# Kernel tuning notes

Hardware: AMD Instinct MI355X
Metric: run time of the kernel (lower is better)

The kernel has to match this reference:

```python
import jax, jax.numpy as jnp
import numpy as np

N_NODES = 100000
N_EDGES = 1600000
F_IN = 64
HID = 64
N_ACT = 8


def gcn_conv(x, edge_index, W, b):
    # PyG GCNConv: h = x @ W; add self-loops; norm = deg^{-1/2}[src]*deg^{-1/2}[dst];
    # out[dst] += norm * h[src]; out += b
    n = x.shape[0]
    h = x @ W  # [N, out]
    row = jnp.concatenate([edge_index[0], jnp.arange(n)])  # src (+ self loops)
    col = jnp.concatenate([edge_index[1], jnp.arange(n)])  # dst (+ self loops)
    deg = jax.ops.segment_sum(jnp.ones_like(col, dtype=h.dtype), col, num_segments=n)
    dinv = jnp.where(deg > 0, jax.lax.rsqrt(deg), 0.0)
    norm = dinv[row] * dinv[col]  # [E+N]
    msg = h[row] * norm[:, None]  # gather + scale
    out = jax.ops.segment_sum(msg, col, num_segments=n)  # scatter-add
    return out + b


def setup_inputs() -> dict:
    key = jax.random.key(0)
    ks = jax.random.split(key, 8)
    x = jax.random.normal(ks[0], (N_NODES, F_IN), dtype=jnp.float32)
    edge_index = jax.random.randint(ks[1], (2, N_EDGES), 0, N_NODES, dtype=jnp.int64)
    def glorot(k, fan_in, fan_out):
        s = jnp.sqrt(6.0 / (fan_in + fan_out))
        return jax.random.uniform(k, (fan_in, fan_out), jnp.float32, -s, s)
    W1 = glorot(ks[2], F_IN, HID)
    b1 = jnp.zeros((HID,), jnp.float32)
    W2 = glorot(ks[3], HID, HID)
    b2 = jnp.zeros((HID,), jnp.float32)
    Wfc = glorot(ks[4], HID, N_ACT)
    bfc = jnp.zeros((N_ACT,), jnp.float32)
    return {"x": x, "edge_index": edge_index, "W1": W1, "b1": b1,
            "W2": W2, "b2": b2, "Wfc": Wfc, "bfc": bfc}


def reference(x, edge_index, W1, b1, W2, b2, Wfc, bfc):
    h = jax.nn.relu(gcn_conv(x, edge_index, W1, b1))
    h = jax.nn.relu(gcn_conv(h, edge_index, W2, b2))
    return h @ Wfc + bfc  # Q-values per node: [N, num_actions]
```

## Files before the change

### kernel.cpp

```cpp
#include <hip/hip_runtime.h>
#include <hip/hip_fp16.h>


#define F 64
#define NACT 8
#define BSH 9
#define BNODES 512
#define CAP 10240
#define EPB 2048
#define HS 67

__global__ __launch_bounds__(256) void k_init(const unsigned int* __restrict__ w,
    int* flag, int* cursor, int E) {
  if (threadIdx.x == 0) *flag = 1;
  cursor[threadIdx.x] = 0;
  __syncthreads();
  int bad = 0;
  for (int i = threadIdx.x; i < 8192; i += 256) {
    if (i < E && w[2 * i + 1] != 0u) bad = 1;
  }
  if (bad) atomicAnd(flag, 0);
}

__device__ __forceinline__ int edge_row(const unsigned int* w, int flag, int e, int E) {
  return flag ? (int)w[2 * e] : (int)w[e];
}
__device__ __forceinline__ int edge_col(const unsigned int* w, int flag, int e, int E) {
  return flag ? (int)w[2 * E + 2 * e] : (int)w[E + e];
}

__global__ __launch_bounds__(256) void k_scatterE(const unsigned int* __restrict__ w,
    const int* __restrict__ flag, int* __restrict__ cursor, unsigned int* __restrict__ slab, int E) {
  __shared__ int hist[256];
  __shared__ int base[256];
  const int tid = threadIdx.x;
  const int fl = *flag;
  hist[tid] = 0;
  __syncthreads();
  int pk[8], bb[8], lr[8];
  const int e0 = blockIdx.x * EPB;
#pragma unroll 8
  for (int j = 0; j < 8; ++j) {
    int e = e0 + j * 256 + tid;
    bb[j] = -1;
    if (e < E) {
      int c = edge_col(w, fl, e, E);
      int s = edge_row(w, fl, e, E);
      int b = c >> BSH;
      pk[j] = (unsigned)s | ((unsigned)(c & (BNODES - 1)) << 17);
      bb[j] = b;
      lr[j] = atomicAdd(&hist[b], 1);
    }
  }
  __syncthreads();
  int h = hist[tid];
  if (h > 0) base[tid] = atomicAdd(&cursor[tid], h);
  __syncthreads();
#pragma unroll 8
  for (int j = 0; j < 8; ++j) {
    if (bb[j] >= 0) {
      slab[(size_t)bb[j] * CAP + base[bb[j]] + lr[j]] = (unsigned)pk[j];
    }
  }
}

__global__ __launch_bounds__(64) void k_slabscan(const int* __restrict__ cursor,
    int* __restrict__ bucketBase, int* __restrict__ csr_off, int NB, int n, int E) {
  int t = threadIdx.x;
  int per = (NB + 63) / 64;
  int base = t * per;
  int local = 0;
  for (int i = 0; i < per; ++i) if (base + i < NB) local += cursor[base + i];
  int inc = local;
  for (int off = 1; off < 64; off <<= 1) {
    int vv = __shfl_up(inc, off);
    if (t >= off) inc += vv;
  }
  int run = inc - local;
  for (int i = 0; i < per; ++i) if (base + i < NB) { bucketBase[base + i] = run; run += cursor[base + i]; }
  if (t == 63) { bucketBase[NB] = inc; csr_off[n] = E; }
}

__global__ __launch_bounds__(256) void k_bucketcsr(const unsigned int* __restrict__ slab,
    const int* __restrict__ bucketBase, int* __restrict__ csr_off, float* __restrict__ dinv,
    int* __restrict__ csr_src, int n) {
  __shared__ int cnt[BNODES];
  __shared__ int off[BNODES];
  __shared__ int sA[256], sB[256];
  const int tid = threadIdx.x;
  const int b = blockIdx.x;
  const int csrbeg = bucketBase[b];
  const int cntb = bucketBase[b + 1] - csrbeg;
  const unsigned int* sl = &slab[(size_t)b * CAP];
  cnt[tid] = 0;
  cnt[tid + 256] = 0;
  __syncthreads();
  for (int i = tid; i < cntb; i += 256) {
    atomicAdd(&cnt[sl[i] >> 17], 1);
  }
  __syncthreads();
  int c0 = cnt[2 * tid], c1 = cnt[2 * tid + 1];
  int p = c0 + c1;
  sA[tid] = p;
  __syncthreads();
  int* srcb = sA;
  int* dstb = sB;
  for (int o = 1; o < 256; o <<= 1) {
    int v = srcb[tid];
    if (tid >= o) v += srcb[tid - o];
    __syncthreads();
    dstb[tid] = v;
    __syncthreads();
    int* t2 = srcb; srcb = dstb; dstb = t2;
  }
  int ex2 = srcb[tid] - p;
  off[2 * tid] = ex2;
  off[2 * tid + 1] = ex2 + c0;
  __syncthreads();
  int v0 = (b << BSH) + 2 * tid;
  if (v0 < n) { csr_off[v0] = csrbeg + off[2 * tid]; dinv[v0] = rsqrtf((float)(c0 + 1)); }
  if (v0 + 1 < n) { csr_off[v0 + 1] = csrbeg + off[2 * tid + 1]; dinv[v0 + 1] = rsqrtf((float)(c1 + 1)); }
  __syncthreads();
  for (int i = tid; i < cntb; i += 256) {
    unsigned int pk = sl[i];
    int dl = pk >> 17;
    int pos = atomicAdd(&off[dl], 1);
    csr_src[csrbeg + pos] = (int)(pk & 0x1FFFFu);
  }
}

__device__ __forceinline__ ushort4 packh4(float a, float b, float c, float d) {
  ushort4 r;
  r.x = __half_as_ushort(__float2half_rn(a));
  r.y = __half_as_ushort(__float2half_rn(b));
  r.z = __half_as_ushort(__float2half_rn(c));
  r.w = __half_as_ushort(__float2half_rn(d));
  return r;
}

__device__ __forceinline__ void accmix(float* a, uint4 g) {
  float one = 1.0f;
  asm volatile(
    "v_fma_mix_f32 %0, %9, %8, %0 op_sel:[0,0,0] op_sel_hi:[1,0,0]\n\t"
    "v_fma_mix_f32 %1, %9, %8, %1 op_sel:[1,0,0] op_sel_hi:[1,0,0]\n\t"
    "v_fma_mix_f32 %2, %10, %8, %2 op_sel:[0,0,0] op_sel_hi:[1,0,0]\n\t"
    "v_fma_mix_f32 %3, %10, %8, %3 op_sel:[1,0,0] op_sel_hi:[1,0,0]\n\t"
    "v_fma_mix_f32 %4, %11, %8, %4 op_sel:[0,0,0] op_sel_hi:[1,0,0]\n\t"
    "v_fma_mix_f32 %5, %11, %8, %5 op_sel:[1,0,0] op_sel_hi:[1,0,0]\n\t"
    "v_fma_mix_f32 %6, %12, %8, %6 op_sel:[0,0,0] op_sel_hi:[1,0,0]\n\t"
    "v_fma_mix_f32 %7, %12, %8, %7 op_sel:[1,0,0] op_sel_hi:[1,0,0]"
    : "+v"(a[0]), "+v"(a[1]), "+v"(a[2]), "+v"(a[3]),
      "+v"(a[4]), "+v"(a[5]), "+v"(a[6]), "+v"(a[7])
    : "v"(one), "v"(g.x), "v"(g.y), "v"(g.z), "v"(g.w));
}

__device__ __forceinline__ void gather8(const uint4* __restrict__ Gv,
    const int* __restrict__ csr_src, int beg, int end, int l, float* a) {
  int j = beg;
  for (; j + 8 <= end; j += 8) {
    uint4 g0 = Gv[(size_t)csr_src[j + 0] * 8 + l];
    uint4 g1 = Gv[(size_t)csr_src[j + 1] * 8 + l];
    uint4 g2 = Gv[(size_t)csr_src[j + 2] * 8 + l];
    uint4 g3 = Gv[(size_t)csr_src[j + 3] * 8 + l];
    uint4 g4 = Gv[(size_t)csr_src[j + 4] * 8 + l];
    uint4 g5 = Gv[(size_t)csr_src[j + 5] * 8 + l];
    uint4 g6 = Gv[(size_t)csr_src[j + 6] * 8 + l];
    uint4 g7 = Gv[(size_t)csr_src[j + 7] * 8 + l];
    accmix(a, g0); accmix(a, g1); accmix(a, g2); accmix(a, g3);
    accmix(a, g4); accmix(a, g5); accmix(a, g6); accmix(a, g7);
  }
  for (; j + 4 <= end; j += 4) {
    uint4 g0 = Gv[(size_t)csr_src[j + 0] * 8 + l];
    uint4 g1 = Gv[(size_t)csr_src[j + 1] * 8 + l];
    uint4 g2 = Gv[(size_t)csr_src[j + 2] * 8 + l];
    uint4 g3 = Gv[(size_t)csr_src[j + 3] * 8 + l];
    accmix(a, g0); accmix(a, g1); accmix(a, g2); accmix(a, g3);
  }
  for (; j < end; ++j) accmix(a, Gv[(size_t)csr_src[j] * 8 + l]);
}

__global__ __launch_bounds__(256) void k_gemm_h(const float* __restrict__ X, const float* __restrict__ W,
    const float* __restrict__ dinv, unsigned short* __restrict__ Gh, int n) {
  __shared__ float xst[F * 68];
  __shared__ float wsh[F * F];
  const int tid = threadIdx.x;
  const int row0 = blockIdx.x * 64;
  for (int i = tid * 4; i < F * F; i += 1024)
    *(float4*)&wsh[i] = *(const float4*)&W[i];
  for (int i = tid * 4; i < 64 * F; i += 1024) {
    int r = i >> 6, k = i & 63;
    float4 v = make_float4(0.f, 0.f, 0.f, 0.f);
    if (row0 + r < n) v = *(const float4*)&X[(size_t)(row0 + r) * F + k];
    xst[(k + 0) * 68 + r] = v.x;
    xst[(k + 1) * 68 + r] = v.y;
    xst[(k + 2) * 68 + r] = v.z;
    xst[(k + 3) * 68 + r] = v.w;
  }
  __syncthreads();
  const int tc = tid & 15;
  const int tr = tid >> 4;
  float a00 = 0.f, a01 = 0.f, a02 = 0.f, a03 = 0.f;
  float a10 = 0.f, a11 = 0.f, a12 = 0.f, a13 = 0.f;
  float a20 = 0.f, a21 = 0.f, a22 = 0.f, a23 = 0.f;
  float a30 = 0.f, a31 = 0.f, a32 = 0.f, a33 = 0.f;
  const float* xp = &xst[tr * 4];
  const float* wp = &wsh[tc * 4];
#pragma unroll 8
  for (int k = 0; k < F; ++k) {
    float4 xv = *(const float4*)&xp[k * 68];
    float4 wv = *(const float4*)&wp[k * F];
    a00 = fmaf(xv.x, wv.x, a00); a01 = fmaf(xv.x, wv.y, a01);
    a02 = fmaf(xv.x, wv.z, a02); a03 = fmaf(xv.x, wv.w, a03);
    a10 = fmaf(xv.y, wv.x, a10); a11 = fmaf(xv.y, wv.y, a11);
    a12 = fmaf(xv.y, wv.z, a12); a13 = fmaf(xv.y, wv.w, a13);
    a20 = fmaf(xv.z, wv.x, a20); a21 = fmaf(xv.z, wv.y, a21);
    a22 = fmaf(xv.z, wv.z, a22); a23 = fmaf(xv.z, wv.w, a23);
    a30 = fmaf(xv.w, wv.x, a30); a31 = fmaf(xv.w, wv.y, a31);
    a32 = fmaf(xv.w, wv.z, a32); a33 = fmaf(xv.w, wv.w, a33);
  }
  const int gc = tc * 4;
  int gr = row0 + tr * 4;
  if (gr + 0 < n) { float d = dinv[gr + 0]; *(ushort4*)&Gh[(size_t)(gr + 0) * F + gc] = packh4(a00 * d, a01 * d, a02 * d, a03 * d); }
  if (gr + 1 < n) { float d = dinv[gr + 1]; *(ushort4*)&Gh[(size_t)(gr + 1) * F + gc] = packh4(a10 * d, a11 * d, a12 * d, a13 * d); }
  if (gr + 2 < n) { float d = dinv[gr + 2]; *(ushort4*)&Gh[(size_t)(gr + 2) * F + gc] = packh4(a20 * d, a21 * d, a22 * d, a23 * d); }
  if (gr + 3 < n) { float d = dinv[gr + 3]; *(ushort4*)&Gh[(size_t)(gr + 3) * F + gc] = packh4(a30 * d, a31 * d, a32 * d, a33 * d); }
}

__global__ __launch_bounds__(512) void k_gather_gemm(const int* __restrict__ csr_off,
    const int* __restrict__ csr_src, const unsigned short* __restrict__ Gh1,
    const float* __restrict__ dinv, const float* __restrict__ bias,
    const float* __restrict__ W2, unsigned short* __restrict__ Gh2, int n) {
  __shared__ float hst[F * HS];
  __shared__ float wsh[F * F];
  const int tid = threadIdx.x;
  const int row0 = blockIdx.x * 64;
  {
    int i = tid * 8;
    *(float4*)&wsh[i] = *(const float4*)&W2[i];
    *(float4*)&wsh[i + 4] = *(const float4*)&W2[i + 4];
  }
  const int ln = tid >> 3;
  const int l = tid & 7;
  const int v = row0 + ln;
  float a[8] = {0.f, 0.f, 0.f, 0.f, 0.f, 0.f, 0.f, 0.f};
  if (v < n) {
    const uint4* Gv = (const uint4*)Gh1;
    accmix(a, Gv[(size_t)v * 8 + l]);
    gather8(Gv, csr_src, csr_off[v], csr_off[v + 1], l, a);
    float d = dinv[v];
#pragma unroll
    for (int jj = 0; jj < 8; ++jj) {
      float h = fmaxf(fmaf(a[jj], d, bias[l * 8 + jj]), 0.f);
      hst[(l * 8 + jj) * HS + ln] = h;
    }
  } else {
#pragma unroll
    for (int jj = 0; jj < 8; ++jj) hst[(l * 8 + jj) * HS + ln] = 0.f;
  }
  __syncthreads();
  const int tc = tid & 15;
  const int tr = tid >> 4;
  const int r0 = 2 * tr;
  float a00 = 0.f, a01 = 0.f, a02 = 0.f, a03 = 0.f;
  float a10 = 0.f, a11 = 0.f, a12 = 0.f, a13 = 0.f;
  const float* wp = &wsh[tc * 4];
#pragma unroll 8
  for (int k = 0; k < F; ++k) {
    float h0 = hst[k * HS + r0];
    float h1 = hst[k * HS + r0 + 1];
    float4 wv = *(const float4*)&wp[k * F];
    a00 = fmaf(h0, wv.x, a00); a01 = fmaf(h0, wv.y, a01);
    a02 = fmaf(h0, wv.z, a02); a03 = fmaf(h0, wv.w, a03);
    a10 = fmaf(h1, wv.x, a10); a11 = fmaf(h1, wv.y, a11);
    a12 = fmaf(h1, wv.z, a12); a13 = fmaf(h1, wv.w, a13);
  }
  const int gc = tc * 4;
  int gr = row0 + r0;
  if (gr < n) { float d = dinv[gr]; *(ushort4*)&Gh2[(size_t)gr * F + gc] = packh4(a00 * d, a01 * d, a02 * d, a03 * d); }
  if (gr + 1 < n) { float d = dinv[gr + 1]; *(ushort4*)&Gh2[(size_t)(gr + 1) * F + gc] = packh4(a10 * d, a11 * d, a12 * d, a13 * d); }
}

__global__ __launch_bounds__(256) void k_gather_fc(const int* __restrict__ csr_off,
    const int* __restrict__ csr_src, const unsigned short* __restrict__ Gh,
    const float* __restrict__ dinv, const float* __restrict__ bias,
    const float* __restrict__ Wfc, const float* __restrict__ bfc,
    float* __restrict__ OUT, int n) {
  __shared__ float wsh[F * 9];
  __shared__ float bs[NACT];
  const int tid = threadIdx.x;
  for (int i = tid; i < F * NACT; i += 256) wsh[(i >> 3) * 9 + (i & 7)] = Wfc[i];
  if (tid < NACT) bs[tid] = bfc[tid];
  __syncthreads();
  int v = blockIdx.x * 32 + (tid >> 3);
  int l = tid & 7;
  if (v >= n) return;
  const uint4* Gv = (const uint4*)Gh;
  float a[8] = {0.f, 0.f, 0.f, 0.f, 0.f, 0.f, 0.f, 0.f};
  accmix(a, Gv[(size_t)v * 8 + l]);
  gather8(Gv, csr_src, csr_off[v], csr_off[v + 1], l, a);
  float d = dinv[v];
  float q[NACT] = {0.f, 0.f, 0.f, 0.f, 0.f, 0.f, 0.f, 0.f};
#pragma unroll
  for (int jj = 0; jj < 8; ++jj) {
    float h = fmaxf(fmaf(a[jj], d, bias[l * 8 + jj]), 0.f);
    const float* wr = &wsh[(l * 8 + jj) * 9];
#pragma unroll
    for (int aa = 0; aa < NACT; ++aa) q[aa] = fmaf(h, wr[aa], q[aa]);
  }
#pragma unroll
  for (int m = 1; m < 8; m <<= 1) {
#pragma unroll
    for (int aa = 0; aa < NACT; ++aa) q[aa] += __shfl_xor(q[aa], m);
  }
  OUT[(size_t)v * NACT + l] = q[l] + bs[l];
}

extern "C" void kernel_launch(void* const* d_in, const int* in_sizes, int n_in,
                              void* d_out, int out_size, void* d_ws, size_t ws_size,
                              hipStream_t stream) {
  const float* x = (const float*)d_in[0];
  const unsigned int* ew = (const unsigned int*)d_in[1];
  const float* W1 = (const float*)d_in[2];
  const float* b1 = (const float*)d_in[3];
  const float* W2 = (const float*)d_in[4];
  const float* b2 = (const float*)d_in[5];
  const float* Wfc = (const float*)d_in[6];
  const float* bfc = (const float*)d_in[7];
  float* out = (float*)d_out;
  const int n = in_sizes[0] / F;
  const int E = in_sizes[1] / 2;
  const int NB = (n + BNODES - 1) >> BSH;

  char* base = (char*)d_ws;
  size_t off = 0;
  auto alloc = [&](size_t bytes) { void* p = base + off; off += (bytes + 255) & ~(size_t)255; return p; };
  int* flag = (int*)alloc(4);
  int* cursor = (int*)alloc(256 * 4);
  int* bucketBase = (int*)alloc((size_t)(NB + 1) * 4);
  int* csr_off = (int*)alloc((size_t)(n + 1) * 4);
  float* dinv = (float*)alloc((size_t)n * 4);
  unsigned int* slab = (unsigned int*)alloc((size_t)NB * CAP * 4);
  int* csr_src = (int*)alloc((size_t)E * 4);
  unsigned short* Gh1 = (unsigned short*)alloc((size_t)n * F * 2);
  unsigned short* Gh2 = (unsigned short*)alloc((size_t)n * F * 2);

  const int gbSc = (E + EPB - 1) / EPB;
  const int gbRow = (n + 63) / 64;
  const int gbGa = (n + 31) / 32;

  hipLaunchKernelGGL(k_init, dim3(1), dim3(256), 0, stream, ew, flag, cursor, E);
  hipLaunchKernelGGL(k_scatterE, dim3(gbSc), dim3(256), 0, stream, ew, flag, cursor, slab, E);
  hipLaunchKernelGGL(k_slabscan, dim3(1), dim3(64), 0, stream, cursor, bucketBase, csr_off, NB, n, E);
  hipLaunchKernelGGL(k_bucketcsr, dim3(NB), dim3(256), 0, stream, slab, bucketBase, csr_off, dinv, csr_src, n);

  hipLaunchKernelGGL(k_gemm_h, dim3(gbRow), dim3(256), 0, stream, x, W1, dinv, Gh1, n);
  hipLaunchKernelGGL(k_gather_gemm, dim3(gbRow), dim3(512), 0, stream, csr_off, csr_src, Gh1, dinv, b1, W2, Gh2, n);
  hipLaunchKernelGGL(k_gather_fc, dim3(gbGa), dim3(256), 0, stream, csr_off, csr_src, Gh2, dinv, b2, Wfc, bfc, out, n);
}
```

Measured before the change: 163.6 us.

## Edge-balanced gather with shared-memory atomics and fold slab scan into bucket CSR

Each gather block now spreads its 64 nodes' incoming edges evenly across its 64 thread groups. It uses a binary search over shared CSR offsets and accumulates partial sums into shared memory with atomics, instead of giving one node to each 8-lane group. This targets load imbalance from varying degrees. The separate single-block scan kernel is removed, and every bucket-CSR block recomputes the prefix over bucket counts itself, saving one launch. The fc gather now uses 512-thread blocks over 64 nodes. The cost is extra shared-memory atomics, extra syncs and fp32 accumulation of the self term via unpacking.

Result: slower. 283.9 us (+73.5%).

```diff
diff --git a/kernel.cpp b/kernel.cpp
--- a/kernel.cpp
+++ b/kernel.cpp
@@ -9,6 +9,7 @@
 #define CAP 10240
 #define EPB 2048
 #define HS 67
+#define ACCS 69
 
 __global__ __launch_bounds__(256) void k_init(const unsigned int* __restrict__ w,
     int* flag, int* cursor, int E) {
@@ -64,44 +65,17 @@
   }
 }
 
-__global__ __launch_bounds__(64) void k_slabscan(const int* __restrict__ cursor,
-    int* __restrict__ bucketBase, int* __restrict__ csr_off, int NB, int n, int E) {
-  int t = threadIdx.x;
-  int per = (NB + 63) / 64;
-  int base = t * per;
-  int local = 0;
-  for (int i = 0; i < per; ++i) if (base + i < NB) local += cursor[base + i];
-  int inc = local;
-  for (int off = 1; off < 64; off <<= 1) {
-    int vv = __shfl_up(inc, off);
-    if (t >= off) inc += vv;
-  }
-  int run = inc - local;
-  for (int i = 0; i < per; ++i) if (base + i < NB) { bucketBase[base + i] = run; run += cursor[base + i]; }
-  if (t == 63) { bucketBase[NB] = inc; csr_off[n] = E; }
-}
-
 __global__ __launch_bounds__(256) void k_bucketcsr(const unsigned int* __restrict__ slab,
-    const int* __restrict__ bucketBase, int* __restrict__ csr_off, float* __restrict__ dinv,
-    int* __restrict__ csr_src, int n) {
+    const int* __restrict__ cursor, int* __restrict__ csr_off, float* __restrict__ dinv,
+    int* __restrict__ csr_src, int n, int NB, int E) {
   __shared__ int cnt[BNODES];
   __shared__ int off[BNODES];
   __shared__ int sA[256], sB[256];
+  __shared__ int sMeta[2];
   const int tid = threadIdx.x;
   const int b = blockIdx.x;
-  const int csrbeg = bucketBase[b];
-  const int cntb = bucketBase[b + 1] - csrbeg;
-  const unsigned int* sl = &slab[(size_t)b * CAP];
-  cnt[tid] = 0;
-  cnt[tid + 256] = 0;
-  __syncthreads();
-  for (int i = tid; i < cntb; i += 256) {
-    atomicAdd(&cnt[sl[i] >> 17], 1);
-  }
-  __syncthreads();
-  int c0 = cnt[2 * tid], c1 = cnt[2 * tid + 1];
-  int p = c0 + c1;
-  sA[tid] = p;
+  int cv = (tid < NB) ? cursor[tid] : 0;
+  sA[tid] = cv;
   __syncthreads();
   int* srcb = sA;
   int* dstb = sB;
@@ -113,6 +87,32 @@
     __syncthreads();
     int* t2 = srcb; srcb = dstb; dstb = t2;
   }
+  if (tid == b) { sMeta[0] = srcb[b] - cv; sMeta[1] = cv; }
+  if (b == 0 && tid == 0) csr_off[n] = E;
+  __syncthreads();
+  const int csrbeg = sMeta[0];
+  const int cntb = sMeta[1];
+  const unsigned int* sl = &slab[(size_t)b * CAP];
+  cnt[tid] = 0;
+  cnt[tid + 256] = 0;
+  __syncthreads();
+  for (int i = tid; i < cntb; i += 256) {
+    atomicAdd(&cnt[sl[i] >> 17], 1);
+  }
+  __syncthreads();
+  int c0 = cnt[2 * tid], c1 = cnt[2 * tid + 1];
+  int p = c0 + c1;
+  sA[tid] = p;
+  __syncthreads();
+  srcb = sA; dstb = sB;
+  for (int o = 1; o < 256; o <<= 1) {
+    int v = srcb[tid];
+    if (tid >= o) v += srcb[tid - o];
+    __syncthreads();
+    dstb[tid] = v;
+    __syncthreads();
+    int* t2 = srcb; srcb = dstb; dstb = t2;
+  }
   int ex2 = srcb[tid] - p;
   off[2 * tid] = ex2;
   off[2 * tid + 1] = ex2 + c0;
@@ -136,6 +136,17 @@
   r.z = __half_as_ushort(__float2half_rn(c));
   r.w = __half_as_ushort(__float2half_rn(d));
   return r;
+}
+
+__device__ __forceinline__ void unpack8(uint4 g, float* f) {
+  union { uint4 u; __half2 h[4]; } u;
+  u.u = g;
+#pragma unroll
+  for (int i = 0; i < 4; ++i) {
+    float2 t = __half22float2(u.h[i]);
+    f[2 * i] = t.x;
+    f[2 * i + 1] = t.y;
+  }
 }
 
 __device__ __forceinline__ void accmix(float* a, uint4 g) {
@@ -154,29 +165,40 @@
     : "v"(one), "v"(g.x), "v"(g.y), "v"(g.z), "v"(g.w));
 }
 
-__device__ __forceinline__ void gather8(const uint4* __restrict__ Gv,
-    const int* __restrict__ csr_src, int beg, int end, int l, float* a) {
-  int j = beg;
-  for (; j + 8 <= end; j += 8) {
-    uint4 g0 = Gv[(size_t)csr_src[j + 0] * 8 + l];
-    uint4 g1 = Gv[(size_t)csr_src[j + 1] * 8 + l];
-    uint4 g2 = Gv[(size_t)csr_src[j + 2] * 8 + l];
-    uint4 g3 = Gv[(size_t)csr_src[j + 3] * 8 + l];
-    uint4 g4 = Gv[(size_t)csr_src[j + 4] * 8 + l];
-    uint4 g5 = Gv[(size_t)csr_src[j + 5] * 8 + l];
-    uint4 g6 = Gv[(size_t)csr_src[j + 6] * 8 + l];
-    uint4 g7 = Gv[(size_t)csr_src[j + 7] * 8 + l];
-    accmix(a, g0); accmix(a, g1); accmix(a, g2); accmix(a, g3);
-    accmix(a, g4); accmix(a, g5); accmix(a, g6); accmix(a, g7);
-  }
-  for (; j + 4 <= end; j += 4) {
-    uint4 g0 = Gv[(size_t)csr_src[j + 0] * 8 + l];
-    uint4 g1 = Gv[(size_t)csr_src[j + 1] * 8 + l];
-    uint4 g2 = Gv[(size_t)csr_src[j + 2] * 8 + l];
-    uint4 g3 = Gv[(size_t)csr_src[j + 3] * 8 + l];
-    accmix(a, g0); accmix(a, g1); accmix(a, g2); accmix(a, g3);
-  }
-  for (; j < end; ++j) accmix(a, Gv[(size_t)csr_src[j] * 8 + l]);
+__device__ __forceinline__ void balanced_gather(const uint4* __restrict__ Gv,
+    const int* __restrict__ csr_src, const int* soff, float* acc, int tid) {
+  const int g = tid >> 3;
+  const int l = tid & 7;
+  const int e0 = soff[0];
+  const int T = soff[64] - e0;
+  int cb = e0 + ((T * g) >> 6);
+  const int ce = e0 + ((T * (g + 1)) >> 6);
+  int lo = 0, hi = 64;
+  while (hi - lo > 1) {
+    int m = (lo + hi) >> 1;
+    if (soff[m] <= cb) lo = m; else hi = m;
+  }
+  int nd = lo;
+  int j = cb;
+  while (j < ce) {
+    int segend = soff[nd + 1];
+    if (segend > ce) segend = ce;
+    if (segend > j) {
+      float a[8] = {0.f, 0.f, 0.f, 0.f, 0.f, 0.f, 0.f, 0.f};
+      for (; j + 4 <= segend; j += 4) {
+        uint4 g0 = Gv[(size_t)csr_src[j + 0] * 8 + l];
+        uint4 g1 = Gv[(size_t)csr_src[j + 1] * 8 + l];
+        uint4 g2 = Gv[(size_t)csr_src[j + 2] * 8 + l];
+        uint4 g3 = Gv[(size_t)csr_src[j + 3] * 8 + l];
+        accmix(a, g0); accmix(a, g1); accmix(a, g2); accmix(a, g3);
+      }
+      for (; j < segend; ++j) accmix(a, Gv[(size_t)csr_src[j] * 8 + l]);
+      float* ap = &acc[nd * ACCS + l * 8];
+#pragma unroll
+      for (int q = 0; q < 8; ++q) atomicAdd(&ap[q], a[q]);
+    }
+    ++nd;
+  }
 }
 
 __global__ __launch_bounds__(256) void k_gemm_h(const float* __restrict__ X, const float* __restrict__ W,
@@ -230,8 +252,10 @@
     const int* __restrict__ csr_src, const unsigned short* __restrict__ Gh1,
     const float* __restrict__ dinv, const float* __restrict__ bias,
     const float* __restrict__ W2, unsigned short* __restrict__ Gh2, int n) {
-  __shared__ float hst[F * HS];
+  __shared__ float buf[64 * ACCS];
   __shared__ float wsh[F * F];
+  __shared__ int soff[65];
+  __shared__ float bsh[64];
   const int tid = threadIdx.x;
   const int row0 = blockIdx.x * 64;
   {
@@ -239,24 +263,36 @@
     *(float4*)&wsh[i] = *(const float4*)&W2[i];
     *(float4*)&wsh[i + 4] = *(const float4*)&W2[i + 4];
   }
-  const int ln = tid >> 3;
+  if (tid < 64) bsh[tid] = bias[tid];
+  if (tid <= 64) {
+    int vv = row0 + tid;
+    soff[tid] = csr_off[vv > n ? n : vv];
+  }
+  const int g = tid >> 3;
   const int l = tid & 7;
-  const int v = row0 + ln;
-  float a[8] = {0.f, 0.f, 0.f, 0.f, 0.f, 0.f, 0.f, 0.f};
-  if (v < n) {
-    const uint4* Gv = (const uint4*)Gh1;
-    accmix(a, Gv[(size_t)v * 8 + l]);
-    gather8(Gv, csr_src, csr_off[v], csr_off[v + 1], l, a);
-    float d = dinv[v];
-#pragma unroll
-    for (int jj = 0; jj < 8; ++jj) {
-      float h = fmaxf(fmaf(a[jj], d, bias[l * 8 + jj]), 0.f);
-      hst[(l * 8 + jj) * HS + ln] = h;
-    }
-  } else {
-#pragma unroll
-    for (int jj = 0; jj < 8; ++jj) hst[(l * 8 + jj) * HS + ln] = 0.f;
-  }
+  const int v = row0 + g;
+  const uint4* Gv = (const uint4*)Gh1;
+  {
+    float fv[8] = {0.f, 0.f, 0.f, 0.f, 0.f, 0.f, 0.f, 0.f};
+    if (v < n) unpack8(Gv[(size_t)v * 8 + l], fv);
+    float* ap = &buf[g * ACCS + l * 8];
+#pragma unroll
+    for (int q = 0; q < 8; ++q) ap[q] = fv[q];
+  }
+  __syncthreads();
+  balanced_gather(Gv, csr_src, soff, buf, tid);
+  __syncthreads();
+  float h[8];
+  {
+    float d = (v < n) ? dinv[v] : 0.f;
+    const float* ap = &buf[g * ACCS + l * 8];
+#pragma unroll
+    for (int q = 0; q < 8; ++q)
+      h[q] = (v < n) ? fmaxf(fmaf(ap[q], d, bsh[l * 8 + q]), 0.f) : 0.f;
+  }
+  __syncthreads();
+#pragma unroll
+  for (int q = 0; q < 8; ++q) buf[(l * 8 + q) * HS + g] = h[q];
   __syncthreads();
   const int tc = tid & 15;
   const int tr = tid >> 4;
@@ -266,8 +302,8 @@
   const float* wp = &wsh[tc * 4];
 #pragma unroll 8
   for (int k = 0; k < F; ++k) {
-    float h0 = hst[k * HS + r0];
-    float h1 = hst[k * HS + r0 + 1];
+    float h0 = buf[k * HS + r0];
+    float h1 = buf[k * HS + r0 + 1];
     float4 wv = *(const float4*)&wp[k * F];
     a00 = fmaf(h0, wv.x, a00); a01 = fmaf(h0, wv.y, a01);
     a02 = fmaf(h0, wv.z, a02); a03 = fmaf(h0, wv.w, a03);
@@ -280,30 +316,47 @@
   if (gr + 1 < n) { float d = dinv[gr + 1]; *(ushort4*)&Gh2[(size_t)(gr + 1) * F + gc] = packh4(a10 * d, a11 * d, a12 * d, a13 * d); }
 }
 
-__global__ __launch_bounds__(256) void k_gather_fc(const int* __restrict__ csr_off,
+__global__ __launch_bounds__(512) void k_gather_fc(const int* __restrict__ csr_off,
     const int* __restrict__ csr_src, const unsigned short* __restrict__ Gh,
     const float* __restrict__ dinv, const float* __restrict__ bias,
     const float* __restrict__ Wfc, const float* __restrict__ bfc,
     float* __restrict__ OUT, int n) {
-  __shared__ float wsh[F * 9];
-  __shared__ float bs[NACT];
+  __shared__ float buf[64 * ACCS];
+  __shared__ float wfc[F * 9];
+  __shared__ int soff[65];
+  __shared__ float bsh[64];
+  __shared__ float bsf[NACT];
   const int tid = threadIdx.x;
-  for (int i = tid; i < F * NACT; i += 256) wsh[(i >> 3) * 9 + (i & 7)] = Wfc[i];
-  if (tid < NACT) bs[tid] = bfc[tid];
-  __syncthreads();
-  int v = blockIdx.x * 32 + (tid >> 3);
-  int l = tid & 7;
+  const int row0 = blockIdx.x * 64;
+  if (tid < F * NACT) wfc[(tid >> 3) * 9 + (tid & 7)] = Wfc[tid];
+  if (tid < 64) bsh[tid] = bias[tid];
+  if (tid < NACT) bsf[tid] = bfc[tid];
+  if (tid <= 64) {
+    int vv = row0 + tid;
+    soff[tid] = csr_off[vv > n ? n : vv];
+  }
+  const int g = tid >> 3;
+  const int l = tid & 7;
+  const int v = row0 + g;
+  const uint4* Gv = (const uint4*)Gh;
+  {
+    float fv[8] = {0.f, 0.f, 0.f, 0.f, 0.f, 0.f, 0.f, 0.f};
+    if (v < n) unpack8(Gv[(size_t)v * 8 + l], fv);
+    float* ap = &buf[g * ACCS + l * 8];
+#pragma unroll
+    for (int q = 0; q < 8; ++q) ap[q] = fv[q];
+  }
+  __syncthreads();
+  balanced_gather(Gv, csr_src, soff, buf, tid);
+  __syncthreads();
   if (v >= n) return;
-  const uint4* Gv = (const uint4*)Gh;
-  float a[8] = {0.f, 0.f, 0.f, 0.f, 0.f, 0.f, 0.f, 0.f};
-  accmix(a, Gv[(size_t)v * 8 + l]);
-  gather8(Gv, csr_src, csr_off[v], csr_off[v + 1], l, a);
   float d = dinv[v];
+  const float* ap = &buf[g * ACCS + l * 8];
   float q[NACT] = {0.f, 0.f, 0.f, 0.f, 0.f, 0.f, 0.f, 0.f};
 #pragma unroll
   for (int jj = 0; jj < 8; ++jj) {
-    float h = fmaxf(fmaf(a[jj], d, bias[l * 8 + jj]), 0.f);
-    const float* wr = &wsh[(l * 8 + jj) * 9];
+    float h = fmaxf(fmaf(ap[jj], d, bsh[l * 8 + jj]), 0.f);
+    const float* wr = &wfc[(l * 8 + jj) * 9];
 #pragma unroll
     for (int aa = 0; aa < NACT; ++aa) q[aa] = fmaf(h, wr[aa], q[aa]);
   }
@@ -312,7 +365,7 @@
 #pragma unroll
     for (int aa = 0; aa < NACT; ++aa) q[aa] += __shfl_xor(q[aa], m);
   }
-  OUT[(size_t)v * NACT + l] = q[l] + bs[l];
+  OUT[(size_t)v * NACT + l] = q[l] + bsf[l];
 }
 
 extern "C" void kernel_launch(void* const* d_in, const int* in_sizes, int n_in,
@@ -336,7 +389,6 @@
   auto alloc = [&](size_t bytes) { void* p = base + off; off += (bytes + 255) & ~(size_t)255; return p; };
   int* flag = (int*)alloc(4);
   int* cursor = (int*)alloc(256 * 4);
-  int* bucketBase = (int*)alloc((size_t)(NB + 1) * 4);
   int* csr_off = (int*)alloc((size_t)(n + 1) * 4);
   float* dinv = (float*)alloc((size_t)n * 4);
   unsigned int* slab = (unsigned int*)alloc((size_t)NB * CAP * 4);
@@ -346,14 +398,12 @@
 
   const int gbSc = (E + EPB - 1) / EPB;
   const int gbRow = (n + 63) / 64;
-  const int gbGa = (n + 31) / 32;
 
   hipLaunchKernelGGL(k_init, dim3(1), dim3(256), 0, stream, ew, flag, cursor, E);
   hipLaunchKernelGGL(k_scatterE, dim3(gbSc), dim3(256), 0, stream, ew, flag, cursor, slab, E);
-  hipLaunchKernelGGL(k_slabscan, dim3(1), dim3(64), 0, stream, cursor, bucketBase, csr_off, NB, n, E);
-  hipLaunchKernelGGL(k_bucketcsr, dim3(NB), dim3(256), 0, stream, slab, bucketBase, csr_off, dinv, csr_src, n);
+  hipLaunchKernelGGL(k_bucketcsr, dim3(NB), dim3(256), 0, stream, slab, cursor, csr_off, dinv, csr_src, n, NB, E);
 
   hipLaunchKernelGGL(k_gemm_h, dim3(gbRow), dim3(256), 0, stream, x, W1, dinv, Gh1, n);
   hipLaunchKernelGGL(k_gather_gemm, dim3(gbRow), dim3(512), 0, stream, csr_off, csr_src, Gh1, dinv, b1, W2, Gh2, n);
-  hipLaunchKernelGGL(k_gather_fc, dim3(gbGa), dim3(256), 0, stream, csr_off, csr_src, Gh2, dinv, b2, Wfc, bfc, out, n);
-}
+  hipLaunchKernelGGL(k_gather_fc, dim3(gbRow), dim3(512), 0, stream, csr_off, csr_src, Gh2, dinv, b2, Wfc, bfc, out, n);
+}
```
